# Kernel tuning notes

Hardware: AMD Instinct MI355X
Metric: run time of the kernel (lower is better)

## Reference

```python
import jax, jax.numpy as jnp
import numpy as np

N_NODES = 50000
N_EDGES = 800000
N_GRAPHS = 512
IN_DIM = 128
HIDDEN = 256
N_CLASSES = 10
MID = 12  # fixed inter-layer dim in TwoConvSAGE


def _segment_mean(x, ids, num_segments):
    s = jax.ops.segment_sum(x, ids, num_segments=num_segments)
    cnt = jax.ops.segment_sum(jnp.ones((x.shape[0],), x.dtype), ids, num_segments=num_segments)
    return jnp.where(cnt[:, None] > 0, s / jnp.maximum(cnt, 1.0)[:, None], 0.0)


def _sage_layer(h, src, dst, Wa, ba, Wb, bb):
    # copy_u + mean: mean over incoming edges of src features
    h_neigh = _segment_mean(h[src], dst, N_NODES)  # [N, d]
    h_total = jnp.concatenate([h, h_neigh], axis=1)  # [N, 2d]
    # nn.Sequential(Linear, Linear) has NO activation in between
    z = (h_total @ Wa + ba) @ Wb + bb
    return jax.nn.relu(z)  # inner F.relu; outer F.relu is idempotent


def setup_inputs() -> dict:
    key = jax.random.key(0)
    ks = jax.random.split(key, 16)
    d = {}
    d['h'] = jax.random.normal(ks[0], (N_NODES, IN_DIM), jnp.float32)
    d['src'] = jax.random.randint(ks[1], (N_EDGES,), 0, N_NODES, jnp.int32)
    d['dst'] = jax.random.randint(ks[2], (N_EDGES,), 0, N_NODES, jnp.int32)
    d['graph_id'] = jnp.sort(jax.random.randint(ks[3], (N_NODES,), 0, N_GRAPHS, jnp.int32))
    s1 = 1.0 / np.sqrt(2 * IN_DIM)
    d['W1a'] = jax.random.uniform(ks[4], (2 * IN_DIM, HIDDEN), jnp.float32, -s1, s1)
    d['b1a'] = jax.random.uniform(ks[5], (HIDDEN,), jnp.float32, -s1, s1)
    s2 = 1.0 / np.sqrt(HIDDEN)
    d['W1b'] = jax.random.uniform(ks[6], (HIDDEN, MID), jnp.float32, -s2, s2)
    d['b1b'] = jax.random.uniform(ks[7], (MID,), jnp.float32, -s2, s2)
    s3 = 1.0 / np.sqrt(2 * MID)
    d['W2a'] = jax.random.uniform(ks[8], (2 * MID, HIDDEN), jnp.float32, -s3, s3)
    d['b2a'] = jax.random.uniform(ks[9], (HIDDEN,), jnp.float32, -s3, s3)
    d['W2b'] = jax.random.uniform(ks[10], (HIDDEN, MID), jnp.float32, -s2, s2)
    d['b2b'] = jax.random.uniform(ks[11], (MID,), jnp.float32, -s2, s2)
    s4 = 1.0 / np.sqrt(MID)
    d['Wc'] = jax.random.uniform(ks[12], (MID, N_CLASSES), jnp.float32, -s4, s4)
    d['bc'] = jax.random.uniform(ks[13], (N_CLASSES,), jnp.float32, -s4, s4)
    return d


def reference(h, src, dst, graph_id, W1a, b1a, W1b, b1b, W2a, b2a, W2b, b2b, Wc, bc):
    h1 = _sage_layer(h, src, dst, W1a, b1a, W1b, b1b)   # [N, 12]
    h2 = _sage_layer(h1, src, dst, W2a, b2a, W2b, b2b)  # [N, 12]
    hg = _segment_mean(h2, graph_id, N_GRAPHS)          # [G, 12]
    return hg @ Wc + bc                                  # [G, n_classes]
```

## Files before the change

### kernel.cpp

```cpp
#include <hip/hip_runtime.h>
#include <hip/hip_bf16.h>

#define NN 50000
#define NE 800000
#define NG 512
#define NB 196
#define B1_CHUNK 2048
#define B1_BLOCKS ((NE + B1_CHUNK - 1) / B1_CHUNK)
#define CAP 5120

typedef unsigned int uint32;
typedef unsigned short ushort16;

__global__ void prep_kernel(const int* __restrict__ dst, int* __restrict__ hist_mat,
                            const float* __restrict__ W1a, const float* __restrict__ b1a,
                            const float* __restrict__ W1b, const float* __restrict__ b1b,
                            const float* __restrict__ W2a, const float* __restrict__ b2a,
                            const float* __restrict__ W2b, const float* __restrict__ b2b,
                            float* __restrict__ W1eff, float* __restrict__ b1eff,
                            float* __restrict__ W2eff, float* __restrict__ b2eff,
                            const int* __restrict__ gid, int* __restrict__ gstart) {
    int bid = blockIdx.x;
    int tid = threadIdx.x;
    if (bid < B1_BLOCKS) {
        __shared__ int hist[NB];
        for (int i = tid; i < NB; i += 256) hist[i] = 0;
        __syncthreads();
        int e0 = bid * B1_CHUNK;
        #pragma unroll
        for (int k = 0; k < 8; ++k) {
            int e = e0 + tid + k * 256;
            if (e < NE) atomicAdd(&hist[dst[e] >> 8], 1);
        }
        __syncthreads();
        int* row = hist_mat + bid * NB;
        for (int i = tid; i < NB; i += 256) row[i] = hist[i];
    } else if (bid < B1_BLOCKS + 14) {
        int t = (bid - B1_BLOCKS) * 256 + tid;
        if (t < 3072) {
            int r = t / 12, c = t % 12;
            float acc = 0.f;
            for (int k = 0; k < 256; ++k) acc += W1a[r*256 + k] * W1b[k*12 + c];
            W1eff[r*12 + c] = acc;
        } else if (t < 3084) {
            int c = t - 3072;
            float acc = b1b[c];
            for (int k = 0; k < 256; ++k) acc += b1a[k] * W1b[k*12 + c];
            b1eff[c] = acc;
        } else if (t < 3372) {
            int u = t - 3084;
            int r = u / 12, c = u % 12;
            float acc = 0.f;
            for (int k = 0; k < 256; ++k) acc += W2a[r*256 + k] * W2b[k*12 + c];
            W2eff[r*12 + c] = acc;
        } else if (t < 3384) {
            int c = t - 3372;
            float acc = b2b[c];
            for (int k = 0; k < 256; ++k) acc += b2a[k] * W2b[k*12 + c];
            b2eff[c] = acc;
        }
    } else {
        int n = (bid - B1_BLOCKS - 14) * 256 + tid;
        if (n < NN) {
            int cur = gid[n];
            int prev = (n == 0) ? -1 : gid[n - 1];
            for (int g = prev + 1; g <= cur; ++g) gstart[g] = n;
            if (n == NN - 1) {
                for (int g = cur + 1; g <= NG; ++g) gstart[g] = NN;
            }
        }
    }
}

__global__ void offs_kernel(const int* __restrict__ hist_mat,
                            int* __restrict__ off_mat, int* __restrict__ btot) {
    __shared__ int sh[512];
    int tid = threadIdx.x;
    int b = blockIdx.x;
    int v = (tid < B1_BLOCKS) ? hist_mat[tid * NB + b] : 0;
    sh[tid] = v;
    __syncthreads();
    for (int off = 1; off < 512; off <<= 1) {
        int t = (tid >= off) ? sh[tid - off] : 0;
        __syncthreads();
        sh[tid] += t;
        __syncthreads();
    }
    if (tid < B1_BLOCKS) off_mat[tid * NB + b] = sh[tid] - v;
    if (tid == B1_BLOCKS - 1) btot[b] = sh[tid];
}

__global__ void place_pairs_kernel(const int* __restrict__ src, const int* __restrict__ dst,
                                   const int* __restrict__ off_mat, const int* __restrict__ btot,
                                   uint32* __restrict__ pairs) {
    __shared__ int sb[256];
    __shared__ int lbase[NB];
    __shared__ int lcur[NB];
    int tid = threadIdx.x;
    int v = (tid < NB) ? btot[tid] : 0;
    sb[tid] = v;
    __syncthreads();
    for (int off = 1; off < 256; off <<= 1) {
        int t = (tid >= off) ? sb[tid - off] : 0;
        __syncthreads();
        sb[tid] += t;
        __syncthreads();
    }
    const int* orow = off_mat + blockIdx.x * NB;
    if (tid < NB) {
        lbase[tid] = (sb[tid] - v) + orow[tid];
        lcur[tid] = 0;
    }
    __syncthreads();
    int e0 = blockIdx.x * B1_CHUNK;
    #pragma unroll
    for (int k = 0; k < 8; ++k) {
        int e = e0 + tid + k * 256;
        if (e < NE) {
            int dd = dst[e];
            int ss = src[e];
            int bb = dd >> 8;
            int idx = atomicAdd(&lcur[bb], 1);
            pairs[lbase[bb] + idx] = ((uint32)ss << 8) | (uint32)(dd & 255);
        }
    }
}

__global__ void p1_kernel(const float* __restrict__ h, const float* __restrict__ W1eff,
                          float* __restrict__ p1t, float* __restrict__ p1b) {
    int n = blockIdx.x * blockDim.x + threadIdx.x;
    if (n >= NN) return;
    const float4* hrow = (const float4*)(h + (size_t)n * 128);
    float acc[24];
    #pragma unroll
    for (int j = 0; j < 24; ++j) acc[j] = 0.f;
    #pragma unroll 4
    for (int kq = 0; kq < 32; ++kq) {
        float4 hv = hrow[kq];
        #pragma unroll
        for (int u = 0; u < 4; ++u) {
            int k = kq * 4 + u;
            float hx = u == 0 ? hv.x : (u == 1 ? hv.y : (u == 2 ? hv.z : hv.w));
            const float4* wt = (const float4*)(W1eff + k * 12);
            const float4* wb = (const float4*)(W1eff + (128 + k) * 12);
            #pragma unroll
            for (int q = 0; q < 3; ++q) {
                float4 a = wt[q];
                float4 b = wb[q];
                acc[q*4 + 0]      += hx * a.x;
                acc[q*4 + 1]      += hx * a.y;
                acc[q*4 + 2]      += hx * a.z;
                acc[q*4 + 3]      += hx * a.w;
                acc[12 + q*4 + 0] += hx * b.x;
                acc[12 + q*4 + 1] += hx * b.y;
                acc[12 + q*4 + 2] += hx * b.z;
                acc[12 + q*4 + 3] += hx * b.w;
            }
        }
    }
    float* pt = p1t + (size_t)n * 12;
    float* pb = p1b + (size_t)n * 12;
    #pragma unroll
    for (int c = 0; c < 12; ++c) pt[c] = acc[c];
    #pragma unroll
    for (int c = 0; c < 12; ++c) pb[c] = acc[12 + c];
}

__global__ void fine_gf1_kernel(const uint32* __restrict__ pairs, const int* __restrict__ btot,
                                const float* __restrict__ p1t, const float* __restrict__ p1b,
                                const float* __restrict__ b1eff, const float* __restrict__ W2eff,
                                int* __restrict__ row_start, ushort16* __restrict__ sorted_src,
                                float* __restrict__ p2t, float* __restrict__ p2b) {
    __shared__ int sb[256];
    __shared__ int cnt[256];
    __shared__ int sc[256];
    __shared__ int rs[257];
    __shared__ float hacc[256 * 13];
    __shared__ float w2[288];
    __shared__ float b1[12];
    __shared__ ushort16 ssrc[CAP];
    int tid = threadIdx.x;
    int b = blockIdx.x;
    if (tid < 256) { sb[tid] = (tid < NB) ? btot[tid] : 0; cnt[tid] = 0; }
    for (int i = tid; i < 288; i += 768) w2[i] = W2eff[i];
    if (tid >= 256 && tid < 268) b1[tid - 256] = b1eff[tid - 256];
    __syncthreads();
    for (int off = 1; off < 256; off <<= 1) {
        int t = (tid < 256 && tid >= off) ? sb[tid - off] : 0;
        __syncthreads();
        if (tid < 256) sb[tid] += t;
        __syncthreads();
    }
    int vb = btot[b];
    int R0 = sb[b] - vb, R1 = R0 + vb;
    bool use_lds = (vb <= CAP);
    for (int i = R0 + tid; i < R1; i += 768)
        atomicAdd(&cnt[(int)(pairs[i] & 255u)], 1);
    __syncthreads();
    if (tid < 256) sc[tid] = cnt[tid];
    __syncthreads();
    for (int off = 1; off < 256; off <<= 1) {
        int t = (tid < 256 && tid >= off) ? sc[tid - off] : 0;
        __syncthreads();
        if (tid < 256) sc[tid] += t;
        __syncthreads();
    }
    if (tid < 256) rs[tid] = R0 + sc[tid] - cnt[tid];
    if (tid == 255) rs[256] = R0 + sc[255];
    __syncthreads();
    if (tid < 256) cnt[tid] = 0;
    int n0 = b << 8;
    int nloc = min(256, NN - n0);
    if (tid < nloc) row_start[n0 + tid] = rs[tid];
    if (b == NB - 1 && tid == 0) row_start[NN] = R1;
    __syncthreads();
    for (int i = R0 + tid; i < R1; i += 768) {
        uint32 pr = pairs[i];
        int ln = (int)(pr & 255u);
        int ss = (int)(pr >> 8);
        int off2 = atomicAdd(&cnt[ln], 1);
        int pos = rs[ln] + off2;
        sorted_src[pos] = (ushort16)ss;
        if (use_lds) ssrc[pos - R0] = (ushort16)ss;
    }
    __syncthreads();
    {
        int li = tid / 3, q = tid - li * 3;
        int r0 = rs[li], r1 = rs[li + 1];
        float4 s = make_float4(0.f, 0.f, 0.f, 0.f);
        if (use_lds) {
            for (int i = r0 - R0; i < r1 - R0; ++i) {
                int sn = (int)ssrc[i];
                float4 v = ((const float4*)(p1b + (size_t)sn * 12))[q];
                s.x += v.x; s.y += v.y; s.z += v.z; s.w += v.w;
            }
        } else {
            for (int i = r0; i < r1; ++i) {
                int sn = (int)sorted_src[i];
                float4 v = ((const float4*)(p1b + (size_t)sn * 12))[q];
                s.x += v.x; s.y += v.y; s.z += v.z; s.w += v.w;
            }
        }
        float* hp = &hacc[li * 13 + q * 4];
        hp[0] = s.x; hp[1] = s.y; hp[2] = s.z; hp[3] = s.w;
    }
    __syncthreads();
    int n = n0 + tid;
    if (tid < 256 && n < NN) {
        int dg = rs[tid + 1] - rs[tid];
        float inv = dg > 0 ? 1.f / (float)dg : 0.f;
        const float4* ptp = (const float4*)(p1t + (size_t)n * 12);
        float4 a0 = ptp[0], a1 = ptp[1], a2 = ptp[2];
        float pt[12] = {a0.x,a0.y,a0.z,a0.w, a1.x,a1.y,a1.z,a1.w, a2.x,a2.y,a2.z,a2.w};
        float h1[12];
        #pragma unroll
        for (int j = 0; j < 12; ++j) {
            float v = pt[j] + hacc[tid * 13 + j] * inv + b1[j];
            h1[j] = v > 0.f ? v : 0.f;
        }
        float oa[12], ob[12];
        #pragma unroll
        for (int co = 0; co < 12; ++co) {
            float A = 0.f, B = 0.f;
            #pragma unroll
            for (int k = 0; k < 12; ++k) {
                A += h1[k] * w2[k*12 + co];
                B += h1[k] * w2[(12+k)*12 + co];
            }
            oa[co] = A; ob[co] = B;
        }
        float4* ot = (float4*)(p2t + (size_t)n * 12);
        float4* ou = (float4*)(p2b + (size_t)n * 12);
        ot[0] = make_float4(oa[0],oa[1],oa[2],oa[3]);
        ot[1] = make_float4(oa[4],oa[5],oa[6],oa[7]);
        ot[2] = make_float4(oa[8],oa[9],oa[10],oa[11]);
        ou[0] = make_float4(ob[0],ob[1],ob[2],ob[3]);
        ou[1] = make_float4(ob[4],ob[5],ob[6],ob[7]);
        ou[2] = make_float4(ob[8],ob[9],ob[10],ob[11]);
    }
}

__global__ void gather_fin2_kernel(const int* __restrict__ row_start,
                                   const ushort16* __restrict__ sorted_src,
                                   const float* __restrict__ p2t, const float* __restrict__ p2b,
                                   const float* __restrict__ b2eff, float* __restrict__ h2) {
    int t = blockIdx.x * blockDim.x + threadIdx.x;
    if (t >= NN * 3) return;
    int n = t / 3, q = t - n * 3;
    int r0 = row_start[n], r1 = row_start[n + 1];
    float4 s = make_float4(0.f, 0.f, 0.f, 0.f);
    for (int i = r0; i < r1; ++i) {
        int sn = (int)sorted_src[i];
        float4 v = ((const float4*)(p2b + (size_t)sn * 12))[q];
        s.x += v.x; s.y += v.y; s.z += v.z; s.w += v.w;
    }
    float inv = (r1 > r0) ? 1.f / (float)(r1 - r0) : 0.f;
    float4 pt = ((const float4*)(p2t + (size_t)n * 12))[q];
    const float* b2 = b2eff + q * 4;
    float4 o;
    o.x = pt.x + s.x * inv + b2[0]; o.x = o.x > 0.f ? o.x : 0.f;
    o.y = pt.y + s.y * inv + b2[1]; o.y = o.y > 0.f ? o.y : 0.f;
    o.z = pt.z + s.z * inv + b2[2]; o.z = o.z > 0.f ? o.z : 0.f;
    o.w = pt.w + s.w * inv + b2[3]; o.w = o.w > 0.f ? o.w : 0.f;
    ((float4*)(h2 + (size_t)n * 12))[q] = o;
}

__global__ void graph_kernel(const float* __restrict__ h2, const int* __restrict__ gstart,
                             const float* __restrict__ Wc, const float* __restrict__ bc,
                             float* __restrict__ out) {
    __shared__ float sh[252];
    __shared__ float hg[12];
    int g = blockIdx.x;
    int r0 = gstart[g], r1 = gstart[g + 1];
    int tid = threadIdx.x;
    int group = tid / 12, ch = tid - group * 12;
    if (tid < 252) {
        float s = 0.f;
        for (int n = r0 + group; n < r1; n += 21) s += h2[(size_t)n * 12 + ch];
        sh[tid] = s;
    }
    __syncthreads();
    if (tid < 12) {
        float tot = 0.f;
        #pragma unroll
        for (int k = 0; k < 21; ++k) tot += sh[k*12 + tid];
        int cntn = r1 - r0;
        hg[tid] = cntn > 0 ? tot / (float)cntn : 0.f;
    }
    __syncthreads();
    if (tid < 10) {
        float o = bc[tid];
        #pragma unroll
        for (int j = 0; j < 12; ++j) o += hg[j] * Wc[j*10 + tid];
        out[g*10 + tid] = o;
    }
}

extern "C" void kernel_launch(void* const* d_in, const int* in_sizes, int n_in,
                              void* d_out, int out_size, void* d_ws, size_t ws_size,
                              hipStream_t stream) {
    const float* h   = (const float*)d_in[0];
    const int* src   = (const int*)d_in[1];
    const int* dst   = (const int*)d_in[2];
    const int* gid   = (const int*)d_in[3];
    const float* W1a = (const float*)d_in[4];
    const float* b1a = (const float*)d_in[5];
    const float* W1b = (const float*)d_in[6];
    const float* b1b = (const float*)d_in[7];
    const float* W2a = (const float*)d_in[8];
    const float* b2a = (const float*)d_in[9];
    const float* W2b = (const float*)d_in[10];
    const float* b2b = (const float*)d_in[11];
    const float* Wc  = (const float*)d_in[12];
    const float* bc  = (const float*)d_in[13];
    float* out = (float*)d_out;

    float* ws = (float*)d_ws;
    float* W1eff = ws;
    float* b1eff = ws + 3072;
    float* W2eff = ws + 3084;
    float* b2eff = ws + 3372;
    float* p1t   = ws + 1000000;
    float* p1b   = ws + 1600000;
    float* p2t   = ws + 2200000;
    float* p2b   = ws + 2800000;
    float* h2    = ws + 3400000;
    uint32* pairs = (uint32*)(ws + 4000000);
    int*   hist_mat   = (int*)(ws + 4800000);
    int*   off_mat    = (int*)(ws + 4880000);
    ushort16* sorted_src = (ushort16*)(ws + 4960000);
    int*   row_start  = (int*)(ws + 5360000);
    int*   btot       = (int*)(ws + 5420000);
    int*   gstart     = (int*)(ws + 5424000);

    prep_kernel<<<B1_BLOCKS + 14 + 196, 256, 0, stream>>>(
        dst, hist_mat, W1a, b1a, W1b, b1b, W2a, b2a, W2b, b2b,
        W1eff, b1eff, W2eff, b2eff, gid, gstart);

    offs_kernel<<<NB, 512, 0, stream>>>(hist_mat, off_mat, btot);

    place_pairs_kernel<<<B1_BLOCKS, 256, 0, stream>>>(src, dst, off_mat, btot, pairs);

    p1_kernel<<<(NN + 255) / 256, 256, 0, stream>>>(h, W1eff, p1t, p1b);

    fine_gf1_kernel<<<NB, 768, 0, stream>>>(pairs, btot, p1t, p1b, b1eff, W2eff,
                                            row_start, sorted_src, p2t, p2b);

    gather_fin2_kernel<<<(NN * 3 + 255) / 256, 256, 0, stream>>>(row_start, sorted_src,
                                                                 p2t, p2b, b2eff, h2);

    graph_kernel<<<NG, 256, 0, stream>>>(h2, gstart, Wc, bc, out);
}
```

Before: 95.77 us.

## Fuse offset scan with p1 projection and fold layer-2 gather into graph pooling

Merges the histogram offset scan with the per-node layer-1 projection into a single 768-thread launch over 196 blocks, so 196*768 threads cover all nodes. It also removes the separate layer-2 gather kernel and the h2 buffer: each graph block now does the neighbour mean, bias and ReLU for its own nodes inside the pooling loop. This cuts two launches and the h2 round trip through memory. The cost is much less parallelism in the layer-2 gather (512 blocks, 252 active threads each, doing scalar loads per channel) and possible load imbalance across graphs.

```diff
diff --git a/kernel.cpp b/kernel.cpp
--- a/kernel.cpp
+++ b/kernel.cpp
@@ -72,22 +72,63 @@
     }
 }
 
-__global__ void offs_kernel(const int* __restrict__ hist_mat,
-                            int* __restrict__ off_mat, int* __restrict__ btot) {
+__global__ void __launch_bounds__(768) offsp1_kernel(
+    const int* __restrict__ hist_mat, int* __restrict__ off_mat, int* __restrict__ btot,
+    const float* __restrict__ h, const float* __restrict__ W1eff,
+    float* __restrict__ p1t, float* __restrict__ p1b) {
     __shared__ int sh[512];
     int tid = threadIdx.x;
     int b = blockIdx.x;
-    int v = (tid < B1_BLOCKS) ? hist_mat[tid * NB + b] : 0;
-    sh[tid] = v;
+    int v = 0;
+    if (tid < 512) {
+        v = (tid < B1_BLOCKS) ? hist_mat[tid * NB + b] : 0;
+        sh[tid] = v;
+    }
     __syncthreads();
     for (int off = 1; off < 512; off <<= 1) {
-        int t = (tid >= off) ? sh[tid - off] : 0;
-        __syncthreads();
-        sh[tid] += t;
+        int t2 = (tid < 512 && tid >= off) ? sh[tid - off] : 0;
+        __syncthreads();
+        if (tid < 512) sh[tid] += t2;
         __syncthreads();
     }
     if (tid < B1_BLOCKS) off_mat[tid * NB + b] = sh[tid] - v;
     if (tid == B1_BLOCKS - 1) btot[b] = sh[tid];
+    int n = b * 768 + tid;
+    if (n >= NN) return;
+    const float4* hrow = (const float4*)(h + (size_t)n * 128);
+    float acc[24];
+    #pragma unroll
+    for (int j = 0; j < 24; ++j) acc[j] = 0.f;
+    #pragma unroll 4
+    for (int kq = 0; kq < 32; ++kq) {
+        float4 hv = hrow[kq];
+        #pragma unroll
+        for (int u = 0; u < 4; ++u) {
+            int k = kq * 4 + u;
+            float hx = u == 0 ? hv.x : (u == 1 ? hv.y : (u == 2 ? hv.z : hv.w));
+            const float4* wt = (const float4*)(W1eff + k * 12);
+            const float4* wb = (const float4*)(W1eff + (128 + k) * 12);
+            #pragma unroll
+            for (int q = 0; q < 3; ++q) {
+                float4 a = wt[q];
+                float4 bq = wb[q];
+                acc[q*4 + 0]      += hx * a.x;
+                acc[q*4 + 1]      += hx * a.y;
+                acc[q*4 + 2]      += hx * a.z;
+                acc[q*4 + 3]      += hx * a.w;
+                acc[12 + q*4 + 0] += hx * bq.x;
+                acc[12 + q*4 + 1] += hx * bq.y;
+                acc[12 + q*4 + 2] += hx * bq.z;
+                acc[12 + q*4 + 3] += hx * bq.w;
+            }
+        }
+    }
+    float* pt = p1t + (size_t)n * 12;
+    float* pb = p1b + (size_t)n * 12;
+    #pragma unroll
+    for (int c = 0; c < 12; ++c) pt[c] = acc[c];
+    #pragma unroll
+    for (int c = 0; c < 12; ++c) pb[c] = acc[12 + c];
 }
 
 __global__ void place_pairs_kernel(const int* __restrict__ src, const int* __restrict__ dst,
@@ -124,46 +165,6 @@
             pairs[lbase[bb] + idx] = ((uint32)ss << 8) | (uint32)(dd & 255);
         }
     }
-}
-
-__global__ void p1_kernel(const float* __restrict__ h, const float* __restrict__ W1eff,
-                          float* __restrict__ p1t, float* __restrict__ p1b) {
-    int n = blockIdx.x * blockDim.x + threadIdx.x;
-    if (n >= NN) return;
-    const float4* hrow = (const float4*)(h + (size_t)n * 128);
-    float acc[24];
-    #pragma unroll
-    for (int j = 0; j < 24; ++j) acc[j] = 0.f;
-    #pragma unroll 4
-    for (int kq = 0; kq < 32; ++kq) {
-        float4 hv = hrow[kq];
-        #pragma unroll
-        for (int u = 0; u < 4; ++u) {
-            int k = kq * 4 + u;
-            float hx = u == 0 ? hv.x : (u == 1 ? hv.y : (u == 2 ? hv.z : hv.w));
-            const float4* wt = (const float4*)(W1eff + k * 12);
-            const float4* wb = (const float4*)(W1eff + (128 + k) * 12);
-            #pragma unroll
-            for (int q = 0; q < 3; ++q) {
-                float4 a = wt[q];
-                float4 b = wb[q];
-                acc[q*4 + 0]      += hx * a.x;
-                acc[q*4 + 1]      += hx * a.y;
-                acc[q*4 + 2]      += hx * a.z;
-                acc[q*4 + 3]      += hx * a.w;
-                acc[12 + q*4 + 0] += hx * b.x;
-                acc[12 + q*4 + 1] += hx * b.y;
-                acc[12 + q*4 + 2] += hx * b.z;
-                acc[12 + q*4 + 3] += hx * b.w;
-            }
-        }
-    }
-    float* pt = p1t + (size_t)n * 12;
-    float* pb = p1b + (size_t)n * 12;
-    #pragma unroll
-    for (int c = 0; c < 12; ++c) pt[c] = acc[c];
-    #pragma unroll
-    for (int c = 0; c < 12; ++c) pb[c] = acc[12 + c];
 }
 
 __global__ void fine_gf1_kernel(const uint32* __restrict__ pairs, const int* __restrict__ btot,
@@ -280,34 +281,12 @@
     }
 }
 
-__global__ void gather_fin2_kernel(const int* __restrict__ row_start,
-                                   const ushort16* __restrict__ sorted_src,
-                                   const float* __restrict__ p2t, const float* __restrict__ p2b,
-                                   const float* __restrict__ b2eff, float* __restrict__ h2) {
-    int t = blockIdx.x * blockDim.x + threadIdx.x;
-    if (t >= NN * 3) return;
-    int n = t / 3, q = t - n * 3;
-    int r0 = row_start[n], r1 = row_start[n + 1];
-    float4 s = make_float4(0.f, 0.f, 0.f, 0.f);
-    for (int i = r0; i < r1; ++i) {
-        int sn = (int)sorted_src[i];
-        float4 v = ((const float4*)(p2b + (size_t)sn * 12))[q];
-        s.x += v.x; s.y += v.y; s.z += v.z; s.w += v.w;
-    }
-    float inv = (r1 > r0) ? 1.f / (float)(r1 - r0) : 0.f;
-    float4 pt = ((const float4*)(p2t + (size_t)n * 12))[q];
-    const float* b2 = b2eff + q * 4;
-    float4 o;
-    o.x = pt.x + s.x * inv + b2[0]; o.x = o.x > 0.f ? o.x : 0.f;
-    o.y = pt.y + s.y * inv + b2[1]; o.y = o.y > 0.f ? o.y : 0.f;
-    o.z = pt.z + s.z * inv + b2[2]; o.z = o.z > 0.f ? o.z : 0.f;
-    o.w = pt.w + s.w * inv + b2[3]; o.w = o.w > 0.f ? o.w : 0.f;
-    ((float4*)(h2 + (size_t)n * 12))[q] = o;
-}
-
-__global__ void graph_kernel(const float* __restrict__ h2, const int* __restrict__ gstart,
-                             const float* __restrict__ Wc, const float* __restrict__ bc,
-                             float* __restrict__ out) {
+__global__ void graph2_kernel(const int* __restrict__ row_start,
+                              const ushort16* __restrict__ sorted_src,
+                              const float* __restrict__ p2t, const float* __restrict__ p2b,
+                              const float* __restrict__ b2eff, const int* __restrict__ gstart,
+                              const float* __restrict__ Wc, const float* __restrict__ bc,
+                              float* __restrict__ out) {
     __shared__ float sh[252];
     __shared__ float hg[12];
     int g = blockIdx.x;
@@ -315,8 +294,17 @@
     int tid = threadIdx.x;
     int group = tid / 12, ch = tid - group * 12;
     if (tid < 252) {
+        float b2c = b2eff[ch];
         float s = 0.f;
-        for (int n = r0 + group; n < r1; n += 21) s += h2[(size_t)n * 12 + ch];
+        for (int n = r0 + group; n < r1; n += 21) {
+            int e0 = row_start[n], e1 = row_start[n + 1];
+            float a = 0.f;
+            for (int i = e0; i < e1; ++i)
+                a += p2b[(size_t)((int)sorted_src[i]) * 12 + ch];
+            float inv = (e1 > e0) ? 1.f / (float)(e1 - e0) : 0.f;
+            float v = p2t[(size_t)n * 12 + ch] + a * inv + b2c;
+            s += v > 0.f ? v : 0.f;
+        }
         sh[tid] = s;
     }
     __syncthreads();
@@ -324,8 +312,8 @@
         float tot = 0.f;
         #pragma unroll
         for (int k = 0; k < 21; ++k) tot += sh[k*12 + tid];
-        int cntn = r1 - r0;
-        hg[tid] = cntn > 0 ? tot / (float)cntn : 0.f;
+        int cn = r1 - r0;
+        hg[tid] = cn > 0 ? tot / (float)cn : 0.f;
     }
     __syncthreads();
     if (tid < 10) {
@@ -364,7 +352,6 @@
     float* p1b   = ws + 1600000;
     float* p2t   = ws + 2200000;
     float* p2b   = ws + 2800000;
-    float* h2    = ws + 3400000;
     uint32* pairs = (uint32*)(ws + 4000000);
     int*   hist_mat   = (int*)(ws + 4800000);
     int*   off_mat    = (int*)(ws + 4880000);
@@ -377,17 +364,13 @@
         dst, hist_mat, W1a, b1a, W1b, b1b, W2a, b2a, W2b, b2b,
         W1eff, b1eff, W2eff, b2eff, gid, gstart);
 
-    offs_kernel<<<NB, 512, 0, stream>>>(hist_mat, off_mat, btot);
+    offsp1_kernel<<<NB, 768, 0, stream>>>(hist_mat, off_mat, btot, h, W1eff, p1t, p1b);
 
     place_pairs_kernel<<<B1_BLOCKS, 256, 0, stream>>>(src, dst, off_mat, btot, pairs);
-
-    p1_kernel<<<(NN + 255) / 256, 256, 0, stream>>>(h, W1eff, p1t, p1b);
 
     fine_gf1_kernel<<<NB, 768, 0, stream>>>(pairs, btot, p1t, p1b, b1eff, W2eff,
                                             row_start, sorted_src, p2t, p2b);
 
-    gather_fin2_kernel<<<(NN * 3 + 255) / 256, 256, 0, stream>>>(row_start, sorted_src,
-                                                                 p2t, p2b, b2eff, h2);
-
-    graph_kernel<<<NG, 256, 0, stream>>>(h2, gstart, Wc, bc, out);
-}
+    graph2_kernel<<<NG, 256, 0, stream>>>(row_start, sorted_src, p2t, p2b, b2eff,
+                                          gstart, Wc, bc, out);
+}
```

After: 124.4 us. 29.8% more time.
